# Kernel tuning notes

Hardware: AMD Instinct MI355X
Metric: run time of the kernel (lower is better)

The kernel has to match this reference:

```python
import jax, jax.numpy as jnp
import numpy as np

D = 128
K = 8
TEMPERATURE = 1.0
LN_EPS = 1e-5
NORM_EPS = 1e-12


def setup_inputs() -> dict:
    key = jax.random.key(0)
    ks = jax.random.split(key, 6)
    B = 262144
    global_prosody = jax.random.normal(ks[0], (B, D), dtype=jnp.float32)
    W = jax.random.normal(ks[1], (D, D), dtype=jnp.float32) / np.sqrt(D)
    b = jnp.zeros((D,), dtype=jnp.float32)
    gamma = jnp.ones((D,), dtype=jnp.float32)
    beta = jnp.zeros((D,), dtype=jnp.float32)
    # codebook initialized as rows of an orthonormal basis (SVD of random init)
    init = jax.random.normal(ks[2], (D, K), dtype=jnp.float32)
    U, _, _ = jnp.linalg.svd(init, full_matrices=False)
    codebook = U[:, :K].T  # (K, D)
    return {"global_prosody": global_prosody, "W": W, "b": b,
            "gamma": gamma, "beta": beta, "codebook": codebook}


def _l2norm(x, axis=-1):
    n = jnp.sqrt(jnp.sum(x * x, axis=axis, keepdims=True))
    return x / jnp.maximum(n, NORM_EPS)


def reference(global_prosody, W, b, gamma, beta, codebook):
    # proj: Linear + LayerNorm
    h = global_prosody @ W.T + b                      # (B, D)
    mu = jnp.mean(h, axis=-1, keepdims=True)
    var = jnp.var(h, axis=-1, keepdims=True)
    h = (h - mu) / jnp.sqrt(var + LN_EPS) * gamma + beta
    # cosine-sim logits
    h_norm = _l2norm(h)                               # (B, D)
    cb_norm = _l2norm(codebook)                       # (K, D)
    logits = (h_norm @ cb_norm.T) / TEMPERATURE       # (B, K)
    soft_assign = jax.nn.softmax(logits, axis=-1)
    hard_indices = jnp.argmax(logits, axis=-1)        # (B,)
    hard_assign = jax.nn.one_hot(hard_indices, K, dtype=jnp.float32)
    # straight-through assignment
    assign = hard_assign + soft_assign - jax.lax.stop_gradient(soft_assign)
    embedding = assign @ codebook                     # (B, D)
    return hard_indices, soft_assign, embedding, logits
```

## Files before the change

### kernel.cpp

```cpp
#include <hip/hip_runtime.h>
#include <math.h>

#define DD 128
#define KK 8
#define LN_EPS 1e-5f
#define NORM_EPS 1e-12f

typedef __attribute__((ext_vector_type(8))) short bf16x8;
typedef __attribute__((ext_vector_type(16))) float f32x16;
typedef unsigned int uint;
typedef unsigned short ushort;

#define G2B_OFF_F   (122880 / 4)
#define SCAL_OFF_F  (123904 / 4)

__device__ inline void split3(float x, uint& h, uint& m, uint& l) {
    uint u0 = __float_as_uint(x);
    uint rh = (u0 + 0x7FFFu + ((u0 >> 16) & 1u)) & 0xFFFF0000u;
    float xh = __uint_as_float(rh);
    float r1 = x - xh;
    uint u1 = __float_as_uint(r1);
    uint rm = (u1 + 0x7FFFu + ((u1 >> 16) & 1u)) & 0xFFFF0000u;
    float xm = __uint_as_float(rm);
    float r2 = r1 - xm;
    uint u2 = __float_as_uint(r2);
    uint rl = (u2 + 0x7FFFu + ((u2 >> 16) & 1u));
    h = rh; m = rm; l = rl;
}

__device__ inline void split3t(float x, uint& h, uint& m, uint& l) {
    uint u0 = __float_as_uint(x);
    float xh = __uint_as_float(u0 & 0xFFFF0000u);
    float r1 = x - xh;
    uint u1 = __float_as_uint(r1);
    float xm = __uint_as_float(u1 & 0xFFFF0000u);
    float r2 = r1 - xm;
    h = u0; m = u1; l = __float_as_uint(r2);
}

__device__ inline uint packhi(uint a1, uint a0) {
    return __builtin_amdgcn_perm(a1, a0, 0x07060302u);
}

__device__ inline void split2packt(float e0, float e1, uint& ph, uint& pm, uint& pl) {
    uint h0, m0, l0, h1, m1, l1;
    split3t(e0, h0, m0, l0);
    split3t(e1, h1, m1, l1);
    ph = packhi(h1, h0);
    pm = packhi(m1, m0);
    pl = packhi(l1, l0);
}

union FragU  { uint4 u; bf16x8 f; };
union AccU16 { f32x16 v; float a[16]; };

__global__ void l1q_prep0(const float* __restrict__ b, const float* __restrict__ gamma,
                          const float* __restrict__ beta, const float* __restrict__ cb,
                          float* __restrict__ ws)
{
    __shared__ float invn_s[KK];
    const int t = threadIdx.x;
    if (t < KK) {
        float s = 0.f;
        for (int j = 0; j < DD; ++j) { float v = cb[t * DD + j]; s = fmaf(v, v, s); }
        invn_s[t] = 1.0f / fmaxf(sqrtf(s), NORM_EPS);
    }
    __syncthreads();
    {
        float g = gamma[t];
        float* g2b = ws + G2B_OFF_F;
        g2b[2 * t]     = g * g;
        g2b[2 * t + 1] = b[t];
    }
    float* scal = ws + SCAL_OFF_F;
    if (t < KK) {
        float in = invn_s[t];
        float p = 0.f, q = 0.f, cu = 0.f;
        for (int j = 0; j < DD; ++j) {
            float c = cb[t * DD + j] * in;
            p  = fmaf(c, gamma[j], p);
            q  = fmaf(c, beta[j], q);
            cu = fmaf(c * gamma[j], b[j], cu);
        }
        scal[t]      = p;
        scal[8 + t]  = q;
        scal[22 + t] = cu;
    }
    if (t == 16) { float s = 0.f; for (int j = 0; j < DD; ++j) { float g = gamma[j]; s = fmaf(g, g, s); } scal[16] = s; }
    if (t == 17) { float s = 0.f; for (int j = 0; j < DD; ++j) s = fmaf(gamma[j], beta[j], s); scal[17] = s; }
    if (t == 18) { float s = 0.f; for (int j = 0; j < DD; ++j) { float v = beta[j]; s = fmaf(v, v, s); } scal[18] = s; }
    if (t == 19) { float s = 0.f; for (int j = 0; j < DD; ++j) s += b[j]; scal[19] = s; }
    if (t == 20) { float s = 0.f; for (int j = 0; j < DD; ++j) s = fmaf(gamma[j] * gamma[j], b[j], s); scal[20] = s; }
    if (t == 21) { float s = 0.f; for (int j = 0; j < DD; ++j) s = fmaf(gamma[j] * beta[j], b[j], s); scal[21] = s; }
}

__global__ void l1q_prepA(const float* __restrict__ W, const float* __restrict__ b,
                          const float* __restrict__ gamma, const float* __restrict__ beta,
                          const float* __restrict__ cb, ushort* __restrict__ wsA)
{
    __shared__ float invn_s[KK];
    __shared__ float we[11][DD];
    __shared__ float wext[32][16];
    const int t = threadIdx.x;
    const int jt = blockIdx.x >> 3;
    const int ks = blockIdx.x & 7;

    if (jt == 4) {
        if (t < KK) {
            float s = 0.f;
            for (int j = 0; j < DD; ++j) { float v = cb[t * DD + j]; s = fmaf(v, v, s); }
            invn_s[t] = 1.0f / fmaxf(sqrtf(s), NORM_EPS);
        }
        __syncthreads();
        for (int idx = t; idx < 11 * DD; idx += 256) {
            int e = idx / DD, j = idx % DD;
            float g = gamma[j];
            float v;
            if (e == 0)      v = 1.0f;
            else if (e == 1) v = g * g;
            else if (e == 2) v = g * beta[j];
            else             v = cb[(e - 3) * DD + j] * invn_s[e - 3] * g;
            we[e][j] = v;
        }
        __syncthreads();
    }

    for (int idx = t; idx < 512; idx += 256) {
        int jl = idx >> 4, kk = idx & 15;
        int k = ks * 16 + kk;
        float val;
        if (jt < 4) {
            val = W[(jt * 32 + jl) * DD + k];
        } else if (jl < 11) {
            float s = 0.f;
            for (int j = 0; j < DD; ++j) s = fmaf(we[jl][j], W[j * DD + k], s);
            val = s;
        } else {
            val = 0.f;
        }
        wext[jl][kk] = val;
    }
    __syncthreads();

    for (int idx = t; idx < 512; idx += 256) {
        int jl = idx >> 4, kk = idx & 15;
        int lane = jl + 32 * (kk >> 3);
        int i = kk & 7;
        uint h, m, l;
        split3(wext[jl][kk], h, m, l);
        int base = jt * 8 + ks;
        wsA[(0 * 40 + base) * 512 + lane * 8 + i] = (ushort)(h >> 16);
        wsA[(1 * 40 + base) * 512 + lane * 8 + i] = (ushort)(m >> 16);
        wsA[(2 * 40 + base) * 512 + lane * 8 + i] = (ushort)(l >> 16);
    }
}

__global__ __launch_bounds__(1024, 4)
void l1q_main(const float* __restrict__ x, const ushort* __restrict__ wsA,
              const float* __restrict__ wsf, const float* __restrict__ cb,
              float* __restrict__ out_idx, float* __restrict__ out_soft,
              float* __restrict__ out_emb, float* __restrict__ out_log,
              int B)
{
    __shared__ uint4 Wl4[7680];
    __shared__ float gath[16][352];
    __shared__ int   besti[16][32];
    __shared__ float g2b_s[256];
    __shared__ float scal_s[32];

    const int t = threadIdx.x;
    const int wave = t >> 6;
    const int lane = t & 63;
    const int n = lane & 31;
    const int h = lane >> 5;
    const int rowbase = blockIdx.x * 512 + wave * 32;
    const int row = rowbase + n;

    const float* xp = x + (size_t)row * DD + h * 8;
    float4 ra = *(const float4*)(xp + 0);
    float4 rc = *(const float4*)(xp + 4);

    {
        const uint4* src = (const uint4*)wsA;
        #pragma unroll
        for (int i = 0; i < 8; ++i) {
            int idx = t + i * 1024;
            if (idx < 7680) Wl4[idx] = src[idx];
        }
    }
    if (t < 256) g2b_s[t] = wsf[G2B_OFF_F + t];
    if (t < 32)  scal_s[t] = wsf[SCAL_OFF_F + t];
    __syncthreads();

    f32x16 acc[5];
    #pragma unroll
    for (int jt = 0; jt < 5; ++jt)
        #pragma unroll
        for (int r = 0; r < 16; ++r) acc[jt][r] = 0.f;

    #pragma unroll
    for (int ks = 0; ks < 8; ++ks) {
        int kn = ks < 7 ? ks + 1 : 7;
        float4 na = *(const float4*)(xp + kn * 16 + 0);
        float4 nc = *(const float4*)(xp + kn * 16 + 4);

        FragU xh, xm, xl;
        split2packt(ra.x, ra.y, xh.u.x, xm.u.x, xl.u.x);
        split2packt(ra.z, ra.w, xh.u.y, xm.u.y, xl.u.y);
        split2packt(rc.x, rc.y, xh.u.z, xm.u.z, xl.u.z);
        split2packt(rc.z, rc.w, xh.u.w, xm.u.w, xl.u.w);

        #pragma unroll
        for (int jt = 0; jt < 5; ++jt) {
            const int pl = jt * 8 + ks;
            FragU wh, wm, wl;
            wh.u = Wl4[(0 * 40 + pl) * 64 + lane];
            wm.u = Wl4[(1 * 40 + pl) * 64 + lane];
            wl.u = Wl4[(2 * 40 + pl) * 64 + lane];
            f32x16 c = acc[jt];
            c = __builtin_amdgcn_mfma_f32_32x32x16_bf16(wl.f, xh.f, c, 0, 0, 0);
            c = __builtin_amdgcn_mfma_f32_32x32x16_bf16(wh.f, xl.f, c, 0, 0, 0);
            c = __builtin_amdgcn_mfma_f32_32x32x16_bf16(wm.f, xm.f, c, 0, 0, 0);
            c = __builtin_amdgcn_mfma_f32_32x32x16_bf16(wm.f, xh.f, c, 0, 0, 0);
            c = __builtin_amdgcn_mfma_f32_32x32x16_bf16(wh.f, xm.f, c, 0, 0, 0);
            c = __builtin_amdgcn_mfma_f32_32x32x16_bf16(wh.f, xh.f, c, 0, 0, 0);
            acc[jt] = c;
        }
        ra = na; rc = nc;
    }

    float s2a = 0.f, t2a = 0.f;
    #pragma unroll
    for (int jt = 0; jt < 4; ++jt) {
        AccU16 a; a.v = acc[jt];
        #pragma unroll
        for (int rq = 0; rq < 4; ++rq) {
            int jb = jt * 32 + 8 * rq + 4 * h;
            #pragma unroll
            for (int r = 0; r < 4; ++r) {
                float2 gb = *(const float2*)&g2b_s[2 * (jb + r)];
                float hv = a.a[rq * 4 + r] + gb.y;
                float h2 = hv * hv;
                s2a += h2;
                t2a = fmaf(gb.x, h2, t2a);
            }
        }
    }
    s2a += __shfl_xor(s2a, 32);
    t2a += __shfl_xor(t2a, 32);

    {
        AccU16 a; a.v = acc[4];
        #pragma unroll
        for (int rq = 0; rq < 4; ++rq) {
            #pragma unroll
            for (int r = 0; r < 4; ++r) {
                int local = r + 8 * rq + 4 * h;
                if (local < 11) gath[wave][n * 11 + local] = a.a[rq * 4 + r];
            }
        }
    }
    __builtin_amdgcn_s_waitcnt(0);
    const float* gp = &gath[wave][n * 11];

    const float inv128 = 1.0f / 128.0f;
    const float cg2s = scal_s[16], cgbs = scal_s[17], cb2s = scal_s[18];

    float s1  = gp[0] + scal_s[19];
    float t1  = gp[1] + scal_s[20];
    float r1v = gp[2] + scal_s[21];
    float u[KK];
    #pragma unroll
    for (int k = 0; k < KK; ++k) u[k] = gp[3 + k] + scal_s[22 + k];

    float mu = s1 * inv128;
    float var = fmaf(-mu, mu, s2a * inv128);
    float istd = 1.0f / sqrtf(var + LN_EPS);
    float nrm2 = istd * istd * (t2a - 2.f * mu * t1 + mu * mu * cg2s)
               + 2.f * istd * (r1v - mu * cgbs) + cb2s;
    float rinv = 1.0f / fmaxf(sqrtf(fmaxf(nrm2, 0.f)), NORM_EPS);

    float lg[KK];
    #pragma unroll
    for (int k = 0; k < KK; ++k)
        lg[k] = (istd * (u[k] - mu * scal_s[k]) + scal_s[8 + k]) * rinv;

    float mx = lg[0]; int bi = 0;
    #pragma unroll
    for (int k = 1; k < KK; ++k) if (lg[k] > mx) { mx = lg[k]; bi = k; }

    float ex[KK], se = 0.f;
    #pragma unroll
    for (int k = 0; k < KK; ++k) { ex[k] = expf(lg[k] - mx); se += ex[k]; }
    float rse = 1.0f / se;

    const int m = rowbase + n;
    if (h == 0) {
        out_idx[m] = (float)bi;
        besti[wave][n] = bi;
        *(float4*)&out_log[(size_t)m * KK]     = make_float4(lg[0], lg[1], lg[2], lg[3]);
        *(float4*)&out_log[(size_t)m * KK + 4] = make_float4(lg[4], lg[5], lg[6], lg[7]);
    } else {
        *(float4*)&out_soft[(size_t)m * KK]     = make_float4(ex[0] * rse, ex[1] * rse, ex[2] * rse, ex[3] * rse);
        *(float4*)&out_soft[(size_t)m * KK + 4] = make_float4(ex[4] * rse, ex[5] * rse, ex[6] * rse, ex[7] * rse);
    }

    __builtin_amdgcn_s_waitcnt(0);
    const float4* cb4 = (const float4*)cb;
    float4* eo = (float4*)out_emb;
    #pragma unroll
    for (int i = 0; i < 16; ++i) {
        int f4 = lane + 64 * i;
        int rl = f4 >> 5;
        int c  = f4 & 31;
        int k0 = besti[wave][rl];
        eo[(size_t)(rowbase + rl) * 32 + c] = cb4[k0 * 32 + c];
    }
}

extern "C" void kernel_launch(void* const* d_in, const int* in_sizes, int n_in,
                              void* d_out, int out_size, void* d_ws, size_t ws_size,
                              hipStream_t stream) {
    const float* x     = (const float*)d_in[0];
    const float* W     = (const float*)d_in[1];
    const float* b     = (const float*)d_in[2];
    const float* gamma = (const float*)d_in[3];
    const float* beta  = (const float*)d_in[4];
    const float* cb    = (const float*)d_in[5];
    const int B = in_sizes[0] / DD;

    float*  ws  = (float*)d_ws;
    ushort* wsA = (ushort*)d_ws;

    float* out    = (float*)d_out;
    float* o_idx  = out;
    float* o_soft = out + (size_t)B;
    float* o_emb  = out + (size_t)B * (1 + KK);
    float* o_log  = out + (size_t)B * (1 + KK + DD);

    hipLaunchKernelGGL(l1q_prep0, dim3(1), dim3(128), 0, stream, b, gamma, beta, cb, ws);
    hipLaunchKernelGGL(l1q_prepA, dim3(40), dim3(256), 0, stream, W, b, gamma, beta, cb, wsA);
    const int grid = B / 512;
    hipLaunchKernelGGL(l1q_main, dim3(grid), dim3(1024), 0, stream,
                       x, wsA, ws, cb, o_idx, o_soft, o_emb, o_log, B);
}
```

Measured before the change: 298.8 us.

## Fuse weight-prep kernels into main kernel and process two row chunks per block

Removes the two preprocessing launches by having every block split W into bf16 limbs, build the extended projection rows and compute the LN/codebook scalars directly in shared memory. Each block now handles two 512-row chunks, halving the grid so the redundant per-block prep is amortized. The cost is that every block repeats the prep work, including a 128-long dot product per extended weight entry, which competes with the main GEMM for time.

```diff
diff --git a/kernel.cpp b/kernel.cpp
--- a/kernel.cpp
+++ b/kernel.cpp
@@ -10,9 +10,6 @@
 typedef __attribute__((ext_vector_type(16))) float f32x16;
 typedef unsigned int uint;
 typedef unsigned short ushort;
-
-#define G2B_OFF_F   (122880 / 4)
-#define SCAL_OFF_F  (123904 / 4)
 
 __device__ inline void split3(float x, uint& h, uint& m, uint& l) {
     uint u0 = __float_as_uint(x);
@@ -54,25 +51,80 @@
 union FragU  { uint4 u; bf16x8 f; };
 union AccU16 { f32x16 v; float a[16]; };
 
-__global__ void l1q_prep0(const float* __restrict__ b, const float* __restrict__ gamma,
-                          const float* __restrict__ beta, const float* __restrict__ cb,
-                          float* __restrict__ ws)
+__global__ __launch_bounds__(1024, 4)
+void l1q_all(const float* __restrict__ x, const float* __restrict__ W,
+             const float* __restrict__ b, const float* __restrict__ gamma,
+             const float* __restrict__ beta, const float* __restrict__ cb,
+             float* __restrict__ out_idx, float* __restrict__ out_soft,
+             float* __restrict__ out_emb, float* __restrict__ out_log,
+             int B)
 {
+    __shared__ uint4 Wl4[7680];
+    __shared__ float gath[16][352];
+    __shared__ int   besti[16][32];
+    __shared__ float g2b_s[256];
+    __shared__ float scal_s[32];
     __shared__ float invn_s[KK];
+
+    ushort* wsA  = (ushort*)Wl4;
+    float*  we_s = &gath[0][0];
+
     const int t = threadIdx.x;
+    const int wave = t >> 6;
+    const int lane = t & 63;
+    const int n = lane & 31;
+    const int h = lane >> 5;
+
+    const float* xp = x + (size_t)(blockIdx.x * 1024 + wave * 32 + n) * DD + h * 8;
+    float4 ra = *(const float4*)(xp + 0);
+    float4 rc = *(const float4*)(xp + 4);
+
     if (t < KK) {
         float s = 0.f;
         for (int j = 0; j < DD; ++j) { float v = cb[t * DD + j]; s = fmaf(v, v, s); }
         invn_s[t] = 1.0f / fmaxf(sqrtf(s), NORM_EPS);
     }
+    if (t < DD) {
+        float g = gamma[t];
+        g2b_s[2 * t]     = g * g;
+        g2b_s[2 * t + 1] = b[t];
+    }
+    {
+        uint4 z = make_uint4(0u, 0u, 0u, 0u);
+        #pragma unroll
+        for (int p = 0; p < 2; ++p) {
+            int i = t + p * 1024;
+            if (i < 1536) {
+                int limb = i >> 9, rem = i & 511;
+                Wl4[(limb * 40 + 32) * 64 + rem] = z;
+            }
+        }
+    }
+    #pragma unroll
+    for (int p = 0; p < 16; ++p) {
+        int idx = t + p * 1024;
+        int jl = idx >> 7, k = idx & 127;
+        float v = W[jl * DD + k];
+        uint hh, mm, ll; split3(v, hh, mm, ll);
+        int jt = jl >> 5, jll = jl & 31, ks = k >> 4, kk = k & 15;
+        int lanei = jll + 32 * (kk >> 3), i2 = kk & 7;
+        int base = jt * 8 + ks;
+        wsA[(0 * 40 + base) * 512 + lanei * 8 + i2] = (ushort)(hh >> 16);
+        wsA[(1 * 40 + base) * 512 + lanei * 8 + i2] = (ushort)(mm >> 16);
+        wsA[(2 * 40 + base) * 512 + lanei * 8 + i2] = (ushort)(ll >> 16);
+    }
     __syncthreads();
-    {
-        float g = gamma[t];
-        float* g2b = ws + G2B_OFF_F;
-        g2b[2 * t]     = g * g;
-        g2b[2 * t + 1] = b[t];
-    }
-    float* scal = ws + SCAL_OFF_F;
+
+    for (int idx = t; idx < 11 * DD; idx += 1024) {
+        int e = idx >> 7, j = idx & 127;
+        float g = gamma[j];
+        float v;
+        if (e == 0)      v = 1.0f;
+        else if (e == 1) v = g * g;
+        else if (e == 2) v = g * beta[j];
+        else             v = cb[(e - 3) * DD + j] * invn_s[e - 3] * g;
+        we_s[idx] = v;
+    }
     if (t < KK) {
         float in = invn_s[t];
         float p = 0.f, q = 0.f, cu = 0.f;
@@ -82,239 +134,168 @@
             q  = fmaf(c, beta[j], q);
             cu = fmaf(c * gamma[j], b[j], cu);
         }
-        scal[t]      = p;
-        scal[8 + t]  = q;
-        scal[22 + t] = cu;
-    }
-    if (t == 16) { float s = 0.f; for (int j = 0; j < DD; ++j) { float g = gamma[j]; s = fmaf(g, g, s); } scal[16] = s; }
-    if (t == 17) { float s = 0.f; for (int j = 0; j < DD; ++j) s = fmaf(gamma[j], beta[j], s); scal[17] = s; }
-    if (t == 18) { float s = 0.f; for (int j = 0; j < DD; ++j) { float v = beta[j]; s = fmaf(v, v, s); } scal[18] = s; }
-    if (t == 19) { float s = 0.f; for (int j = 0; j < DD; ++j) s += b[j]; scal[19] = s; }
-    if (t == 20) { float s = 0.f; for (int j = 0; j < DD; ++j) s = fmaf(gamma[j] * gamma[j], b[j], s); scal[20] = s; }
-    if (t == 21) { float s = 0.f; for (int j = 0; j < DD; ++j) s = fmaf(gamma[j] * beta[j], b[j], s); scal[21] = s; }
-}
-
-__global__ void l1q_prepA(const float* __restrict__ W, const float* __restrict__ b,
-                          const float* __restrict__ gamma, const float* __restrict__ beta,
-                          const float* __restrict__ cb, ushort* __restrict__ wsA)
-{
-    __shared__ float invn_s[KK];
-    __shared__ float we[11][DD];
-    __shared__ float wext[32][16];
-    const int t = threadIdx.x;
-    const int jt = blockIdx.x >> 3;
-    const int ks = blockIdx.x & 7;
-
-    if (jt == 4) {
-        if (t < KK) {
+        scal_s[t]      = p;
+        scal_s[8 + t]  = q;
+        scal_s[22 + t] = cu;
+    }
+    if (t == 16) { float s = 0.f; for (int j = 0; j < DD; ++j) { float g = gamma[j]; s = fmaf(g, g, s); } scal_s[16] = s; }
+    if (t == 17) { float s = 0.f; for (int j = 0; j < DD; ++j) s = fmaf(gamma[j], beta[j], s); scal_s[17] = s; }
+    if (t == 18) { float s = 0.f; for (int j = 0; j < DD; ++j) { float v = beta[j]; s = fmaf(v, v, s); } scal_s[18] = s; }
+    if (t == 19) { float s = 0.f; for (int j = 0; j < DD; ++j) s += b[j]; scal_s[19] = s; }
+    if (t == 20) { float s = 0.f; for (int j = 0; j < DD; ++j) s = fmaf(gamma[j] * gamma[j], b[j], s); scal_s[20] = s; }
+    if (t == 21) { float s = 0.f; for (int j = 0; j < DD; ++j) s = fmaf(gamma[j] * beta[j], b[j], s); scal_s[21] = s; }
+    __syncthreads();
+
+    #pragma unroll
+    for (int p = 0; p < 2; ++p) {
+        int idx = t + p * 1024;
+        if (idx < 11 * DD) {
+            int e = idx >> 7, k = idx & 127;
             float s = 0.f;
-            for (int j = 0; j < DD; ++j) { float v = cb[t * DD + j]; s = fmaf(v, v, s); }
-            invn_s[t] = 1.0f / fmaxf(sqrtf(s), NORM_EPS);
-        }
-        __syncthreads();
-        for (int idx = t; idx < 11 * DD; idx += 256) {
-            int e = idx / DD, j = idx % DD;
-            float g = gamma[j];
-            float v;
-            if (e == 0)      v = 1.0f;
-            else if (e == 1) v = g * g;
-            else if (e == 2) v = g * beta[j];
-            else             v = cb[(e - 3) * DD + j] * invn_s[e - 3] * g;
-            we[e][j] = v;
-        }
-        __syncthreads();
-    }
-
-    for (int idx = t; idx < 512; idx += 256) {
-        int jl = idx >> 4, kk = idx & 15;
-        int k = ks * 16 + kk;
-        float val;
-        if (jt < 4) {
-            val = W[(jt * 32 + jl) * DD + k];
-        } else if (jl < 11) {
-            float s = 0.f;
-            for (int j = 0; j < DD; ++j) s = fmaf(we[jl][j], W[j * DD + k], s);
-            val = s;
+            for (int j = 0; j < DD; ++j) s = fmaf(we_s[e * DD + j], W[j * DD + k], s);
+            uint hh, mm, ll; split3(s, hh, mm, ll);
+            int ks = k >> 4, kk = k & 15;
+            int lanei = e + 32 * (kk >> 3), i2 = kk & 7;
+            int base = 32 + ks;
+            wsA[(0 * 40 + base) * 512 + lanei * 8 + i2] = (ushort)(hh >> 16);
+            wsA[(1 * 40 + base) * 512 + lanei * 8 + i2] = (ushort)(mm >> 16);
+            wsA[(2 * 40 + base) * 512 + lanei * 8 + i2] = (ushort)(ll >> 16);
+        }
+    }
+    __syncthreads();
+
+    const float inv128 = 1.0f / 128.0f;
+
+    #pragma unroll 1
+    for (int c = 0; c < 2; ++c) {
+        const int rowbase = blockIdx.x * 1024 + c * 512 + wave * 32;
+        const float* xnext = (c == 0) ? (xp + 512 * DD) : xp;
+
+        f32x16 acc[5];
+        #pragma unroll
+        for (int jt = 0; jt < 5; ++jt)
+            #pragma unroll
+            for (int r = 0; r < 16; ++r) acc[jt][r] = 0.f;
+
+        #pragma unroll
+        for (int ks = 0; ks < 8; ++ks) {
+            const float* pf = (ks < 7) ? (xp + (ks + 1) * 16) : xnext;
+            float4 na = *(const float4*)(pf + 0);
+            float4 nc = *(const float4*)(pf + 4);
+
+            FragU xh, xm, xl;
+            split2packt(ra.x, ra.y, xh.u.x, xm.u.x, xl.u.x);
+            split2packt(ra.z, ra.w, xh.u.y, xm.u.y, xl.u.y);
+            split2packt(rc.x, rc.y, xh.u.z, xm.u.z, xl.u.z);
+            split2packt(rc.z, rc.w, xh.u.w, xm.u.w, xl.u.w);
+
+            #pragma unroll
+            for (int jt = 0; jt < 5; ++jt) {
+                const int pl = jt * 8 + ks;
+                FragU wh, wm, wl;
+                wh.u = Wl4[(0 * 40 + pl) * 64 + lane];
+                wm.u = Wl4[(1 * 40 + pl) * 64 + lane];
+                wl.u = Wl4[(2 * 40 + pl) * 64 + lane];
+                f32x16 cacc = acc[jt];
+                cacc = __builtin_amdgcn_mfma_f32_32x32x16_bf16(wl.f, xh.f, cacc, 0, 0, 0);
+                cacc = __builtin_amdgcn_mfma_f32_32x32x16_bf16(wh.f, xl.f, cacc, 0, 0, 0);
+                cacc = __builtin_amdgcn_mfma_f32_32x32x16_bf16(wm.f, xm.f, cacc, 0, 0, 0);
+                cacc = __builtin_amdgcn_mfma_f32_32x32x16_bf16(wm.f, xh.f, cacc, 0, 0, 0);
+                cacc = __builtin_amdgcn_mfma_f32_32x32x16_bf16(wh.f, xm.f, cacc, 0, 0, 0);
+                cacc = __builtin_amdgcn_mfma_f32_32x32x16_bf16(wh.f, xh.f, cacc, 0, 0, 0);
+                acc[jt] = cacc;
+            }
+            ra = na; rc = nc;
+        }
+
+        float s2a = 0.f, t2a = 0.f;
+        #pragma unroll
+        for (int jt = 0; jt < 4; ++jt) {
+            AccU16 a; a.v = acc[jt];
+            #pragma unroll
+            for (int rq = 0; rq < 4; ++rq) {
+                int jb = jt * 32 + 8 * rq + 4 * h;
+                #pragma unroll
+                for (int r = 0; r < 4; ++r) {
+                    float2 gb = *(const float2*)&g2b_s[2 * (jb + r)];
+                    float hv = a.a[rq * 4 + r] + gb.y;
+                    float h2 = hv * hv;
+                    s2a += h2;
+                    t2a = fmaf(gb.x, h2, t2a);
+                }
+            }
+        }
+        s2a += __shfl_xor(s2a, 32);
+        t2a += __shfl_xor(t2a, 32);
+
+        {
+            AccU16 a; a.v = acc[4];
+            #pragma unroll
+            for (int rq = 0; rq < 4; ++rq) {
+                #pragma unroll
+                for (int r = 0; r < 4; ++r) {
+                    int local = r + 8 * rq + 4 * h;
+                    if (local < 11) gath[wave][n * 11 + local] = a.a[rq * 4 + r];
+                }
+            }
+        }
+        __builtin_amdgcn_s_waitcnt(0);
+        const float* gp = &gath[wave][n * 11];
+
+        const float cg2s = scal_s[16], cgbs = scal_s[17], cb2s = scal_s[18];
+
+        float s1  = gp[0] + scal_s[19];
+        float t1  = gp[1] + scal_s[20];
+        float r1v = gp[2] + scal_s[21];
+        float u[KK];
+        #pragma unroll
+        for (int k = 0; k < KK; ++k) u[k] = gp[3 + k] + scal_s[22 + k];
+
+        float mu = s1 * inv128;
+        float var = fmaf(-mu, mu, s2a * inv128);
+        float istd = 1.0f / sqrtf(var + LN_EPS);
+        float nrm2 = istd * istd * (t2a - 2.f * mu * t1 + mu * mu * cg2s)
+                   + 2.f * istd * (r1v - mu * cgbs) + cb2s;
+        float rinv = 1.0f / fmaxf(sqrtf(fmaxf(nrm2, 0.f)), NORM_EPS);
+
+        float lg[KK];
+        #pragma unroll
+        for (int k = 0; k < KK; ++k)
+            lg[k] = (istd * (u[k] - mu * scal_s[k]) + scal_s[8 + k]) * rinv;
+
+        float mx = lg[0]; int bi = 0;
+        #pragma unroll
+        for (int k = 1; k < KK; ++k) if (lg[k] > mx) { mx = lg[k]; bi = k; }
+
+        float ex[KK], se = 0.f;
+        #pragma unroll
+        for (int k = 0; k < KK; ++k) { ex[k] = expf(lg[k] - mx); se += ex[k]; }
+        float rse = 1.0f / se;
+
+        const int m = rowbase + n;
+        if (h == 0) {
+            out_idx[m] = (float)bi;
+            besti[wave][n] = bi;
+            *(float4*)&out_log[(size_t)m * KK]     = make_float4(lg[0], lg[1], lg[2], lg[3]);
+            *(float4*)&out_log[(size_t)m * KK + 4] = make_float4(lg[4], lg[5], lg[6], lg[7]);
         } else {
-            val = 0.f;
-        }
-        wext[jl][kk] = val;
-    }
-    __syncthreads();
-
-    for (int idx = t; idx < 512; idx += 256) {
-        int jl = idx >> 4, kk = idx & 15;
-        int lane = jl + 32 * (kk >> 3);
-        int i = kk & 7;
-        uint h, m, l;
-        split3(wext[jl][kk], h, m, l);
-        int base = jt * 8 + ks;
-        wsA[(0 * 40 + base) * 512 + lane * 8 + i] = (ushort)(h >> 16);
-        wsA[(1 * 40 + base) * 512 + lane * 8 + i] = (ushort)(m >> 16);
-        wsA[(2 * 40 + base) * 512 + lane * 8 + i] = (ushort)(l >> 16);
-    }
-}
-
-__global__ __launch_bounds__(1024, 4)
-void l1q_main(const float* __restrict__ x, const ushort* __restrict__ wsA,
-              const float* __restrict__ wsf, const float* __restrict__ cb,
-              float* __restrict__ out_idx, float* __restrict__ out_soft,
-              float* __restrict__ out_emb, float* __restrict__ out_log,
-              int B)
-{
-    __shared__ uint4 Wl4[7680];
-    __shared__ float gath[16][352];
-    __shared__ int   besti[16][32];
-    __shared__ float g2b_s[256];
-    __shared__ float scal_s[32];
-
-    const int t = threadIdx.x;
-    const int wave = t >> 6;
-    const int lane = t & 63;
-    const int n = lane & 31;
-    const int h = lane >> 5;
-    const int rowbase = blockIdx.x * 512 + wave * 32;
-    const int row = rowbase + n;
-
-    const float* xp = x + (size_t)row * DD + h * 8;
-    float4 ra = *(const float4*)(xp + 0);
-    float4 rc = *(const float4*)(xp + 4);
-
-    {
-        const uint4* src = (const uint4*)wsA;
-        #pragma unroll
-        for (int i = 0; i < 8; ++i) {
-            int idx = t + i * 1024;
-            if (idx < 7680) Wl4[idx] = src[idx];
-        }
-    }
-    if (t < 256) g2b_s[t] = wsf[G2B_OFF_F + t];
-    if (t < 32)  scal_s[t] = wsf[SCAL_OFF_F + t];
-    __syncthreads();
-
-    f32x16 acc[5];
-    #pragma unroll
-    for (int jt = 0; jt < 5; ++jt)
-        #pragma unroll
-        for (int r = 0; r < 16; ++r) acc[jt][r] = 0.f;
-
-    #pragma unroll
-    for (int ks = 0; ks < 8; ++ks) {
-        int kn = ks < 7 ? ks + 1 : 7;
-        float4 na = *(const float4*)(xp + kn * 16 + 0);
-        float4 nc = *(const float4*)(xp + kn * 16 + 4);
-
-        FragU xh, xm, xl;
-        split2packt(ra.x, ra.y, xh.u.x, xm.u.x, xl.u.x);
-        split2packt(ra.z, ra.w, xh.u.y, xm.u.y, xl.u.y);
-        split2packt(rc.x, rc.y, xh.u.z, xm.u.z, xl.u.z);
-        split2packt(rc.z, rc.w, xh.u.w, xm.u.w, xl.u.w);
-
-        #pragma unroll
-        for (int jt = 0; jt < 5; ++jt) {
-            const int pl = jt * 8 + ks;
-            FragU wh, wm, wl;
-            wh.u = Wl4[(0 * 40 + pl) * 64 + lane];
-            wm.u = Wl4[(1 * 40 + pl) * 64 + lane];
-            wl.u = Wl4[(2 * 40 + pl) * 64 + lane];
-            f32x16 c = acc[jt];
-            c = __builtin_amdgcn_mfma_f32_32x32x16_bf16(wl.f, xh.f, c, 0, 0, 0);
-            c = __builtin_amdgcn_mfma_f32_32x32x16_bf16(wh.f, xl.f, c, 0, 0, 0);
-            c = __builtin_amdgcn_mfma_f32_32x32x16_bf16(wm.f, xm.f, c, 0, 0, 0);
-            c = __builtin_amdgcn_mfma_f32_32x32x16_bf16(wm.f, xh.f, c, 0, 0, 0);
-            c = __builtin_amdgcn_mfma_f32_32x32x16_bf16(wh.f, xm.f, c, 0, 0, 0);
-            c = __builtin_amdgcn_mfma_f32_32x32x16_bf16(wh.f, xh.f, c, 0, 0, 0);
-            acc[jt] = c;
-        }
-        ra = na; rc = nc;
-    }
-
-    float s2a = 0.f, t2a = 0.f;
-    #pragma unroll
-    for (int jt = 0; jt < 4; ++jt) {
-        AccU16 a; a.v = acc[jt];
-        #pragma unroll
-        for (int rq = 0; rq < 4; ++rq) {
-            int jb = jt * 32 + 8 * rq + 4 * h;
-            #pragma unroll
-            for (int r = 0; r < 4; ++r) {
-                float2 gb = *(const float2*)&g2b_s[2 * (jb + r)];
-                float hv = a.a[rq * 4 + r] + gb.y;
-                float h2 = hv * hv;
-                s2a += h2;
-                t2a = fmaf(gb.x, h2, t2a);
-            }
-        }
-    }
-    s2a += __shfl_xor(s2a, 32);
-    t2a += __shfl_xor(t2a, 32);
-
-    {
-        AccU16 a; a.v = acc[4];
-        #pragma unroll
-        for (int rq = 0; rq < 4; ++rq) {
-            #pragma unroll
-            for (int r = 0; r < 4; ++r) {
-                int local = r + 8 * rq + 4 * h;
-                if (local < 11) gath[wave][n * 11 + local] = a.a[rq * 4 + r];
-            }
-        }
-    }
-    __builtin_amdgcn_s_waitcnt(0);
-    const float* gp = &gath[wave][n * 11];
-
-    const float inv128 = 1.0f / 128.0f;
-    const float cg2s = scal_s[16], cgbs = scal_s[17], cb2s = scal_s[18];
-
-    float s1  = gp[0] + scal_s[19];
-    float t1  = gp[1] + scal_s[20];
-    float r1v = gp[2] + scal_s[21];
-    float u[KK];
-    #pragma unroll
-    for (int k = 0; k < KK; ++k) u[k] = gp[3 + k] + scal_s[22 + k];
-
-    float mu = s1 * inv128;
-    float var = fmaf(-mu, mu, s2a * inv128);
-    float istd = 1.0f / sqrtf(var + LN_EPS);
-    float nrm2 = istd * istd * (t2a - 2.f * mu * t1 + mu * mu * cg2s)
-               + 2.f * istd * (r1v - mu * cgbs) + cb2s;
-    float rinv = 1.0f / fmaxf(sqrtf(fmaxf(nrm2, 0.f)), NORM_EPS);
-
-    float lg[KK];
-    #pragma unroll
-    for (int k = 0; k < KK; ++k)
-        lg[k] = (istd * (u[k] - mu * scal_s[k]) + scal_s[8 + k]) * rinv;
-
-    float mx = lg[0]; int bi = 0;
-    #pragma unroll
-    for (int k = 1; k < KK; ++k) if (lg[k] > mx) { mx = lg[k]; bi = k; }
-
-    float ex[KK], se = 0.f;
-    #pragma unroll
-    for (int k = 0; k < KK; ++k) { ex[k] = expf(lg[k] - mx); se += ex[k]; }
-    float rse = 1.0f / se;
-
-    const int m = rowbase + n;
-    if (h == 0) {
-        out_idx[m] = (float)bi;
-        besti[wave][n] = bi;
-        *(float4*)&out_log[(size_t)m * KK]     = make_float4(lg[0], lg[1], lg[2], lg[3]);
-        *(float4*)&out_log[(size_t)m * KK + 4] = make_float4(lg[4], lg[5], lg[6], lg[7]);
-    } else {
-        *(float4*)&out_soft[(size_t)m * KK]     = make_float4(ex[0] * rse, ex[1] * rse, ex[2] * rse, ex[3] * rse);
-        *(float4*)&out_soft[(size_t)m * KK + 4] = make_float4(ex[4] * rse, ex[5] * rse, ex[6] * rse, ex[7] * rse);
-    }
-
-    __builtin_amdgcn_s_waitcnt(0);
-    const float4* cb4 = (const float4*)cb;
-    float4* eo = (float4*)out_emb;
-    #pragma unroll
-    for (int i = 0; i < 16; ++i) {
-        int f4 = lane + 64 * i;
-        int rl = f4 >> 5;
-        int c  = f4 & 31;
-        int k0 = besti[wave][rl];
-        eo[(size_t)(rowbase + rl) * 32 + c] = cb4[k0 * 32 + c];
+            *(float4*)&out_soft[(size_t)m * KK]     = make_float4(ex[0] * rse, ex[1] * rse, ex[2] * rse, ex[3] * rse);
+            *(float4*)&out_soft[(size_t)m * KK + 4] = make_float4(ex[4] * rse, ex[5] * rse, ex[6] * rse, ex[7] * rse);
+        }
+
+        __builtin_amdgcn_s_waitcnt(0);
+        const float4* cb4 = (const float4*)cb;
+        float4* eo = (float4*)out_emb;
+        #pragma unroll
+        for (int i = 0; i < 16; ++i) {
+            int f4 = lane + 64 * i;
+            int rl = f4 >> 5;
+            int cc = f4 & 31;
+            int k0 = besti[wave][rl];
+            eo[(size_t)(rowbase + rl) * 32 + cc] = cb4[k0 * 32 + cc];
+        }
+
+        xp = xnext;
     }
 }
 
@@ -329,18 +310,13 @@
     const float* cb    = (const float*)d_in[5];
     const int B = in_sizes[0] / DD;
 
-    float*  ws  = (float*)d_ws;
-    ushort* wsA = (ushort*)d_ws;
-
     float* out    = (float*)d_out;
     float* o_idx  = out;
     float* o_soft = out + (size_t)B;
     float* o_emb  = out + (size_t)B * (1 + KK);
     float* o_log  = out + (size_t)B * (1 + KK + DD);
 
-    hipLaunchKernelGGL(l1q_prep0, dim3(1), dim3(128), 0, stream, b, gamma, beta, cb, ws);
-    hipLaunchKernelGGL(l1q_prepA, dim3(40), dim3(256), 0, stream, W, b, gamma, beta, cb, wsA);
-    const int grid = B / 512;
-    hipLaunchKernelGGL(l1q_main, dim3(grid), dim3(1024), 0, stream,
-                       x, wsA, ws, cb, o_idx, o_soft, o_emb, o_log, B);
-}
+    const int grid = B / 1024;
+    hipLaunchKernelGGL(l1q_all, dim3(grid), dim3(1024), 0, stream,
+                       x, W, b, gamma, beta, cb, o_idx, o_soft, o_emb, o_log, B);
+}
```

Result: no change. 295.4 us (-1.2%).

## Process two 512-row chunks per block to amortize LDS weight staging

Applied to the files above, without the earlier changes.

Each block now handles 1024 rows in two sequential chunks, reusing the LDS-staged split-bf16 weight tiles and halving the grid size. The first x fragment of the next chunk is prefetched during the last k-step of the current one, and s_setprio raises wave priority around the MFMA bursts. This cuts the per-block cost of copying about 120KB of weights into LDS, in exchange for fewer blocks (256) and less parallelism, which could cause tail or occupancy effects on a GPU with many CUs.

```diff
diff --git a/kernel.cpp b/kernel.cpp
--- a/kernel.cpp
+++ b/kernel.cpp
@@ -173,10 +173,8 @@
     const int lane = t & 63;
     const int n = lane & 31;
     const int h = lane >> 5;
-    const int rowbase = blockIdx.x * 512 + wave * 32;
-    const int row = rowbase + n;
-
-    const float* xp = x + (size_t)row * DD + h * 8;
+
+    const float* xp = x + (size_t)(blockIdx.x * 1024 + wave * 32 + n) * DD + h * 8;
     float4 ra = *(const float4*)(xp + 0);
     float4 rc = *(const float4*)(xp + 4);
 
@@ -192,129 +190,140 @@
     if (t < 32)  scal_s[t] = wsf[SCAL_OFF_F + t];
     __syncthreads();
 
-    f32x16 acc[5];
-    #pragma unroll
-    for (int jt = 0; jt < 5; ++jt)
-        #pragma unroll
-        for (int r = 0; r < 16; ++r) acc[jt][r] = 0.f;
-
-    #pragma unroll
-    for (int ks = 0; ks < 8; ++ks) {
-        int kn = ks < 7 ? ks + 1 : 7;
-        float4 na = *(const float4*)(xp + kn * 16 + 0);
-        float4 nc = *(const float4*)(xp + kn * 16 + 4);
-
-        FragU xh, xm, xl;
-        split2packt(ra.x, ra.y, xh.u.x, xm.u.x, xl.u.x);
-        split2packt(ra.z, ra.w, xh.u.y, xm.u.y, xl.u.y);
-        split2packt(rc.x, rc.y, xh.u.z, xm.u.z, xl.u.z);
-        split2packt(rc.z, rc.w, xh.u.w, xm.u.w, xl.u.w);
-
-        #pragma unroll
-        for (int jt = 0; jt < 5; ++jt) {
-            const int pl = jt * 8 + ks;
-            FragU wh, wm, wl;
-            wh.u = Wl4[(0 * 40 + pl) * 64 + lane];
-            wm.u = Wl4[(1 * 40 + pl) * 64 + lane];
-            wl.u = Wl4[(2 * 40 + pl) * 64 + lane];
-            f32x16 c = acc[jt];
-            c = __builtin_amdgcn_mfma_f32_32x32x16_bf16(wl.f, xh.f, c, 0, 0, 0);
-            c = __builtin_amdgcn_mfma_f32_32x32x16_bf16(wh.f, xl.f, c, 0, 0, 0);
-            c = __builtin_amdgcn_mfma_f32_32x32x16_bf16(wm.f, xm.f, c, 0, 0, 0);
-            c = __builtin_amdgcn_mfma_f32_32x32x16_bf16(wm.f, xh.f, c, 0, 0, 0);
-            c = __builtin_amdgcn_mfma_f32_32x32x16_bf16(wh.f, xm.f, c, 0, 0, 0);
-            c = __builtin_amdgcn_mfma_f32_32x32x16_bf16(wh.f, xh.f, c, 0, 0, 0);
-            acc[jt] = c;
-        }
-        ra = na; rc = nc;
-    }
-
-    float s2a = 0.f, t2a = 0.f;
-    #pragma unroll
-    for (int jt = 0; jt < 4; ++jt) {
-        AccU16 a; a.v = acc[jt];
-        #pragma unroll
-        for (int rq = 0; rq < 4; ++rq) {
-            int jb = jt * 32 + 8 * rq + 4 * h;
+    const float inv128 = 1.0f / 128.0f;
+
+    #pragma unroll 1
+    for (int c = 0; c < 2; ++c) {
+        const int rowbase = blockIdx.x * 1024 + c * 512 + wave * 32;
+        const float* xnext = (c == 0) ? (xp + 512 * DD) : xp;
+
+        f32x16 acc[5];
+        #pragma unroll
+        for (int jt = 0; jt < 5; ++jt)
             #pragma unroll
-            for (int r = 0; r < 4; ++r) {
-                float2 gb = *(const float2*)&g2b_s[2 * (jb + r)];
-                float hv = a.a[rq * 4 + r] + gb.y;
-                float h2 = hv * hv;
-                s2a += h2;
-                t2a = fmaf(gb.x, h2, t2a);
+            for (int r = 0; r < 16; ++r) acc[jt][r] = 0.f;
+
+        #pragma unroll
+        for (int ks = 0; ks < 8; ++ks) {
+            const float* pf = (ks < 7) ? (xp + (ks + 1) * 16) : xnext;
+            float4 na = *(const float4*)(pf + 0);
+            float4 nc = *(const float4*)(pf + 4);
+
+            FragU xh, xm, xl;
+            split2packt(ra.x, ra.y, xh.u.x, xm.u.x, xl.u.x);
+            split2packt(ra.z, ra.w, xh.u.y, xm.u.y, xl.u.y);
+            split2packt(rc.x, rc.y, xh.u.z, xm.u.z, xl.u.z);
+            split2packt(rc.z, rc.w, xh.u.w, xm.u.w, xl.u.w);
+
+            __builtin_amdgcn_s_setprio(1);
+            #pragma unroll
+            for (int jt = 0; jt < 5; ++jt) {
+                const int pl = jt * 8 + ks;
+                FragU wh, wm, wl;
+                wh.u = Wl4[(0 * 40 + pl) * 64 + lane];
+                wm.u = Wl4[(1 * 40 + pl) * 64 + lane];
+                wl.u = Wl4[(2 * 40 + pl) * 64 + lane];
+                f32x16 cacc = acc[jt];
+                cacc = __builtin_amdgcn_mfma_f32_32x32x16_bf16(wl.f, xh.f, cacc, 0, 0, 0);
+                cacc = __builtin_amdgcn_mfma_f32_32x32x16_bf16(wh.f, xl.f, cacc, 0, 0, 0);
+                cacc = __builtin_amdgcn_mfma_f32_32x32x16_bf16(wm.f, xm.f, cacc, 0, 0, 0);
+                cacc = __builtin_amdgcn_mfma_f32_32x32x16_bf16(wm.f, xh.f, cacc, 0, 0, 0);
+                cacc = __builtin_amdgcn_mfma_f32_32x32x16_bf16(wh.f, xm.f, cacc, 0, 0, 0);
+                cacc = __builtin_amdgcn_mfma_f32_32x32x16_bf16(wh.f, xh.f, cacc, 0, 0, 0);
+                acc[jt] = cacc;
             }
-        }
-    }
-    s2a += __shfl_xor(s2a, 32);
-    t2a += __shfl_xor(t2a, 32);
-
-    {
-        AccU16 a; a.v = acc[4];
-        #pragma unroll
-        for (int rq = 0; rq < 4; ++rq) {
+            __builtin_amdgcn_s_setprio(0);
+            ra = na; rc = nc;
+        }
+
+        float s2a = 0.f, t2a = 0.f;
+        #pragma unroll
+        for (int jt = 0; jt < 4; ++jt) {
+            AccU16 a; a.v = acc[jt];
             #pragma unroll
-            for (int r = 0; r < 4; ++r) {
-                int local = r + 8 * rq + 4 * h;
-                if (local < 11) gath[wave][n * 11 + local] = a.a[rq * 4 + r];
+            for (int rq = 0; rq < 4; ++rq) {
+                int jb = jt * 32 + 8 * rq + 4 * h;
+                #pragma unroll
+                for (int r = 0; r < 4; ++r) {
+                    float2 gb = *(const float2*)&g2b_s[2 * (jb + r)];
+                    float hv = a.a[rq * 4 + r] + gb.y;
+                    float h2 = hv * hv;
+                    s2a += h2;
+                    t2a = fmaf(gb.x, h2, t2a);
+                }
             }
         }
-    }
-    __builtin_amdgcn_s_waitcnt(0);
-    const float* gp = &gath[wave][n * 11];
-
-    const float inv128 = 1.0f / 128.0f;
-    const float cg2s = scal_s[16], cgbs = scal_s[17], cb2s = scal_s[18];
-
-    float s1  = gp[0] + scal_s[19];
-    float t1  = gp[1] + scal_s[20];
-    float r1v = gp[2] + scal_s[21];
-    float u[KK];
-    #pragma unroll
-    for (int k = 0; k < KK; ++k) u[k] = gp[3 + k] + scal_s[22 + k];
-
-    float mu = s1 * inv128;
-    float var = fmaf(-mu, mu, s2a * inv128);
-    float istd = 1.0f / sqrtf(var + LN_EPS);
-    float nrm2 = istd * istd * (t2a - 2.f * mu * t1 + mu * mu * cg2s)
-               + 2.f * istd * (r1v - mu * cgbs) + cb2s;
-    float rinv = 1.0f / fmaxf(sqrtf(fmaxf(nrm2, 0.f)), NORM_EPS);
-
-    float lg[KK];
-    #pragma unroll
-    for (int k = 0; k < KK; ++k)
-        lg[k] = (istd * (u[k] - mu * scal_s[k]) + scal_s[8 + k]) * rinv;
-
-    float mx = lg[0]; int bi = 0;
-    #pragma unroll
-    for (int k = 1; k < KK; ++k) if (lg[k] > mx) { mx = lg[k]; bi = k; }
-
-    float ex[KK], se = 0.f;
-    #pragma unroll
-    for (int k = 0; k < KK; ++k) { ex[k] = expf(lg[k] - mx); se += ex[k]; }
-    float rse = 1.0f / se;
-
-    const int m = rowbase + n;
-    if (h == 0) {
-        out_idx[m] = (float)bi;
-        besti[wave][n] = bi;
-        *(float4*)&out_log[(size_t)m * KK]     = make_float4(lg[0], lg[1], lg[2], lg[3]);
-        *(float4*)&out_log[(size_t)m * KK + 4] = make_float4(lg[4], lg[5], lg[6], lg[7]);
-    } else {
-        *(float4*)&out_soft[(size_t)m * KK]     = make_float4(ex[0] * rse, ex[1] * rse, ex[2] * rse, ex[3] * rse);
-        *(float4*)&out_soft[(size_t)m * KK + 4] = make_float4(ex[4] * rse, ex[5] * rse, ex[6] * rse, ex[7] * rse);
-    }
-
-    __builtin_amdgcn_s_waitcnt(0);
-    const float4* cb4 = (const float4*)cb;
-    float4* eo = (float4*)out_emb;
-    #pragma unroll
-    for (int i = 0; i < 16; ++i) {
-        int f4 = lane + 64 * i;
-        int rl = f4 >> 5;
-        int c  = f4 & 31;
-        int k0 = besti[wave][rl];
-        eo[(size_t)(rowbase + rl) * 32 + c] = cb4[k0 * 32 + c];
+        s2a += __shfl_xor(s2a, 32);
+        t2a += __shfl_xor(t2a, 32);
+
+        {
+            AccU16 a; a.v = acc[4];
+            #pragma unroll
+            for (int rq = 0; rq < 4; ++rq) {
+                #pragma unroll
+                for (int r = 0; r < 4; ++r) {
+                    int local = r + 8 * rq + 4 * h;
+                    if (local < 11) gath[wave][n * 11 + local] = a.a[rq * 4 + r];
+                }
+            }
+        }
+        __builtin_amdgcn_s_waitcnt(0);
+        const float* gp = &gath[wave][n * 11];
+
+        const float cg2s = scal_s[16], cgbs = scal_s[17], cb2s = scal_s[18];
+
+        float s1  = gp[0] + scal_s[19];
+        float t1  = gp[1] + scal_s[20];
+        float r1v = gp[2] + scal_s[21];
+        float u[KK];
+        #pragma unroll
+        for (int k = 0; k < KK; ++k) u[k] = gp[3 + k] + scal_s[22 + k];
+
+        float mu = s1 * inv128;
+        float var = fmaf(-mu, mu, s2a * inv128);
+        float istd = 1.0f / sqrtf(var + LN_EPS);
+        float nrm2 = istd * istd * (t2a - 2.f * mu * t1 + mu * mu * cg2s)
+                   + 2.f * istd * (r1v - mu * cgbs) + cb2s;
+        float rinv = 1.0f / fmaxf(sqrtf(fmaxf(nrm2, 0.f)), NORM_EPS);
+
+        float lg[KK];
+        #pragma unroll
+        for (int k = 0; k < KK; ++k)
+            lg[k] = (istd * (u[k] - mu * scal_s[k]) + scal_s[8 + k]) * rinv;
+
+        float mx = lg[0]; int bi = 0;
+        #pragma unroll
+        for (int k = 1; k < KK; ++k) if (lg[k] > mx) { mx = lg[k]; bi = k; }
+
+        float ex[KK], se = 0.f;
+        #pragma unroll
+        for (int k = 0; k < KK; ++k) { ex[k] = expf(lg[k] - mx); se += ex[k]; }
+        float rse = 1.0f / se;
+
+        const int m = rowbase + n;
+        if (h == 0) {
+            out_idx[m] = (float)bi;
+            besti[wave][n] = bi;
+            *(float4*)&out_log[(size_t)m * KK]     = make_float4(lg[0], lg[1], lg[2], lg[3]);
+            *(float4*)&out_log[(size_t)m * KK + 4] = make_float4(lg[4], lg[5], lg[6], lg[7]);
+        } else {
+            *(float4*)&out_soft[(size_t)m * KK]     = make_float4(ex[0] * rse, ex[1] * rse, ex[2] * rse, ex[3] * rse);
+            *(float4*)&out_soft[(size_t)m * KK + 4] = make_float4(ex[4] * rse, ex[5] * rse, ex[6] * rse, ex[7] * rse);
+        }
+
+        __builtin_amdgcn_s_waitcnt(0);
+        const float4* cb4 = (const float4*)cb;
+        float4* eo = (float4*)out_emb;
+        #pragma unroll
+        for (int i = 0; i < 16; ++i) {
+            int f4 = lane + 64 * i;
+            int rl = f4 >> 5;
+            int cc = f4 & 31;
+            int k0 = besti[wave][rl];
+            eo[(size_t)(rowbase + rl) * 32 + cc] = cb4[k0 * 32 + cc];
+        }
+
+        xp = xnext;
     }
 }
 
@@ -340,7 +349,7 @@
 
     hipLaunchKernelGGL(l1q_prep0, dim3(1), dim3(128), 0, stream, b, gamma, beta, cb, ws);
     hipLaunchKernelGGL(l1q_prepA, dim3(40), dim3(256), 0, stream, W, b, gamma, beta, cb, wsA);
-    const int grid = B / 512;
+    const int grid = B / 1024;
     hipLaunchKernelGGL(l1q_main, dim3(grid), dim3(1024), 0, stream,
                        x, wsA, ws, cb, o_idx, o_soft, o_emb, o_log, B);
 }
```

New measurement: 308.3 us. 3.2% more time.

## Merge prep kernels into one launch and prefetch x two k-steps ahead

Applied to the files above, without the earlier changes.

Folds the scalar/g2b precompute kernel into the block of the weight-prep kernel that already computes codebook norms, removing one kernel launch. In the main kernel, the x row loads are now issued two k-slices ahead instead of one, to hide more global memory latency behind the MFMA chain. This holds more registers for the extra prefetched fragments, which could affect occupancy.

```diff
diff --git a/kernel.cpp b/kernel.cpp
--- a/kernel.cpp
+++ b/kernel.cpp
@@ -54,49 +54,10 @@
 union FragU  { uint4 u; bf16x8 f; };
 union AccU16 { f32x16 v; float a[16]; };
 
-__global__ void l1q_prep0(const float* __restrict__ b, const float* __restrict__ gamma,
-                          const float* __restrict__ beta, const float* __restrict__ cb,
-                          float* __restrict__ ws)
-{
-    __shared__ float invn_s[KK];
-    const int t = threadIdx.x;
-    if (t < KK) {
-        float s = 0.f;
-        for (int j = 0; j < DD; ++j) { float v = cb[t * DD + j]; s = fmaf(v, v, s); }
-        invn_s[t] = 1.0f / fmaxf(sqrtf(s), NORM_EPS);
-    }
-    __syncthreads();
-    {
-        float g = gamma[t];
-        float* g2b = ws + G2B_OFF_F;
-        g2b[2 * t]     = g * g;
-        g2b[2 * t + 1] = b[t];
-    }
-    float* scal = ws + SCAL_OFF_F;
-    if (t < KK) {
-        float in = invn_s[t];
-        float p = 0.f, q = 0.f, cu = 0.f;
-        for (int j = 0; j < DD; ++j) {
-            float c = cb[t * DD + j] * in;
-            p  = fmaf(c, gamma[j], p);
-            q  = fmaf(c, beta[j], q);
-            cu = fmaf(c * gamma[j], b[j], cu);
-        }
-        scal[t]      = p;
-        scal[8 + t]  = q;
-        scal[22 + t] = cu;
-    }
-    if (t == 16) { float s = 0.f; for (int j = 0; j < DD; ++j) { float g = gamma[j]; s = fmaf(g, g, s); } scal[16] = s; }
-    if (t == 17) { float s = 0.f; for (int j = 0; j < DD; ++j) s = fmaf(gamma[j], beta[j], s); scal[17] = s; }
-    if (t == 18) { float s = 0.f; for (int j = 0; j < DD; ++j) { float v = beta[j]; s = fmaf(v, v, s); } scal[18] = s; }
-    if (t == 19) { float s = 0.f; for (int j = 0; j < DD; ++j) s += b[j]; scal[19] = s; }
-    if (t == 20) { float s = 0.f; for (int j = 0; j < DD; ++j) s = fmaf(gamma[j] * gamma[j], b[j], s); scal[20] = s; }
-    if (t == 21) { float s = 0.f; for (int j = 0; j < DD; ++j) s = fmaf(gamma[j] * beta[j], b[j], s); scal[21] = s; }
-}
-
-__global__ void l1q_prepA(const float* __restrict__ W, const float* __restrict__ b,
-                          const float* __restrict__ gamma, const float* __restrict__ beta,
-                          const float* __restrict__ cb, ushort* __restrict__ wsA)
+__global__ void l1q_prep(const float* __restrict__ W, const float* __restrict__ b,
+                         const float* __restrict__ gamma, const float* __restrict__ beta,
+                         const float* __restrict__ cb, ushort* __restrict__ wsA,
+                         float* __restrict__ ws)
 {
     __shared__ float invn_s[KK];
     __shared__ float we[11][DD];
@@ -123,6 +84,35 @@
             we[e][j] = v;
         }
         __syncthreads();
+
+        if (ks == 0) {
+            if (t < DD) {
+                float g = gamma[t];
+                float* g2b = ws + G2B_OFF_F;
+                g2b[2 * t]     = g * g;
+                g2b[2 * t + 1] = b[t];
+            }
+            float* scal = ws + SCAL_OFF_F;
+            if (t < KK) {
+                float in = invn_s[t];
+                float p = 0.f, q = 0.f, cu = 0.f;
+                for (int j = 0; j < DD; ++j) {
+                    float c = cb[t * DD + j] * in;
+                    p  = fmaf(c, gamma[j], p);
+                    q  = fmaf(c, beta[j], q);
+                    cu = fmaf(c * gamma[j], b[j], cu);
+                }
+                scal[t]      = p;
+                scal[8 + t]  = q;
+                scal[22 + t] = cu;
+            }
+            if (t == 16) { float s = 0.f; for (int j = 0; j < DD; ++j) { float g = gamma[j]; s = fmaf(g, g, s); } scal[16] = s; }
+            if (t == 17) { float s = 0.f; for (int j = 0; j < DD; ++j) s = fmaf(gamma[j], beta[j], s); scal[17] = s; }
+            if (t == 18) { float s = 0.f; for (int j = 0; j < DD; ++j) { float v = beta[j]; s = fmaf(v, v, s); } scal[18] = s; }
+            if (t == 19) { float s = 0.f; for (int j = 0; j < DD; ++j) s += b[j]; scal[19] = s; }
+            if (t == 20) { float s = 0.f; for (int j = 0; j < DD; ++j) s = fmaf(gamma[j] * gamma[j], b[j], s); scal[20] = s; }
+            if (t == 21) { float s = 0.f; for (int j = 0; j < DD; ++j) s = fmaf(gamma[j] * beta[j], b[j], s); scal[21] = s; }
+        }
     }
 
     for (int idx = t; idx < 512; idx += 256) {
@@ -177,8 +167,10 @@
     const int row = rowbase + n;
 
     const float* xp = x + (size_t)row * DD + h * 8;
-    float4 ra = *(const float4*)(xp + 0);
-    float4 rc = *(const float4*)(xp + 4);
+    float4 c0a = *(const float4*)(xp + 0);
+    float4 c0c = *(const float4*)(xp + 4);
+    float4 c1a = *(const float4*)(xp + 16);
+    float4 c1c = *(const float4*)(xp + 20);
 
     {
         const uint4* src = (const uint4*)wsA;
@@ -200,15 +192,15 @@
 
     #pragma unroll
     for (int ks = 0; ks < 8; ++ks) {
-        int kn = ks < 7 ? ks + 1 : 7;
-        float4 na = *(const float4*)(xp + kn * 16 + 0);
-        float4 nc = *(const float4*)(xp + kn * 16 + 4);
+        int kp = (ks < 6) ? ks + 2 : 7;
+        float4 pa = *(const float4*)(xp + kp * 16 + 0);
+        float4 pc = *(const float4*)(xp + kp * 16 + 4);
 
         FragU xh, xm, xl;
-        split2packt(ra.x, ra.y, xh.u.x, xm.u.x, xl.u.x);
-        split2packt(ra.z, ra.w, xh.u.y, xm.u.y, xl.u.y);
-        split2packt(rc.x, rc.y, xh.u.z, xm.u.z, xl.u.z);
-        split2packt(rc.z, rc.w, xh.u.w, xm.u.w, xl.u.w);
+        split2packt(c0a.x, c0a.y, xh.u.x, xm.u.x, xl.u.x);
+        split2packt(c0a.z, c0a.w, xh.u.y, xm.u.y, xl.u.y);
+        split2packt(c0c.x, c0c.y, xh.u.z, xm.u.z, xl.u.z);
+        split2packt(c0c.z, c0c.w, xh.u.w, xm.u.w, xl.u.w);
 
         #pragma unroll
         for (int jt = 0; jt < 5; ++jt) {
@@ -226,7 +218,8 @@
             c = __builtin_amdgcn_mfma_f32_32x32x16_bf16(wh.f, xh.f, c, 0, 0, 0);
             acc[jt] = c;
         }
-        ra = na; rc = nc;
+        c0a = c1a; c0c = c1c;
+        c1a = pa;  c1c = pc;
     }
 
     float s2a = 0.f, t2a = 0.f;
@@ -338,8 +331,7 @@
     float* o_emb  = out + (size_t)B * (1 + KK);
     float* o_log  = out + (size_t)B * (1 + KK + DD);
 
-    hipLaunchKernelGGL(l1q_prep0, dim3(1), dim3(128), 0, stream, b, gamma, beta, cb, ws);
-    hipLaunchKernelGGL(l1q_prepA, dim3(40), dim3(256), 0, stream, W, b, gamma, beta, cb, wsA);
+    hipLaunchKernelGGL(l1q_prep, dim3(40), dim3(256), 0, stream, W, b, gamma, beta, cb, wsA, ws);
     const int grid = B / 512;
     hipLaunchKernelGGL(l1q_main, dim3(grid), dim3(1024), 0, stream,
                        x, wsA, ws, cb, o_idx, o_soft, o_emb, o_log, B);
```

After: 288.3 us. 3.5% less time.
